# Performance work log

Hardware: AMD Instinct MI355X
Metric: run time of the kernel (lower is better)

## Reference

```python
import jax, jax.numpy as jnp
import numpy as np

BLOCK = 128
EPS = 1e-5

def _fp8_dequant_weight(w, s):
    # s: [out//128, in//128] per-block scales. Expand to full weight shape.
    sb = jnp.repeat(jnp.repeat(s, BLOCK, axis=0), BLOCK, axis=1)  # [out, in]
    # fake fp8 quantize: scale down, cast to e4m3, cast back, scale up
    wq = (w / sb).astype(jnp.float8_e4m3fn).astype(jnp.float32)
    return wq * sb

def _fp8_linear(x, w, s):
    return x @ _fp8_dequant_weight(w, s).T  # [N, out]

def _layernorm(h, gamma, beta):
    mu = jnp.mean(h, axis=-1, keepdims=True)
    var = jnp.mean(jnp.square(h - mu), axis=-1, keepdims=True)
    return (h - mu) * jax.lax.rsqrt(var + EPS) * gamma + beta

def setup_inputs() -> dict:
    key = jax.random.key(0)
    ks = jax.random.split(key, 4)
    H, LO, SO, N = 4096, 8192, 2048, 8192
    return {
        "x": jax.random.normal(ks[0], (N, H), dtype=jnp.float32),
        "w_a": jax.random.normal(ks[1], (LO, H), dtype=jnp.float32),
        "s_a": jnp.ones((LO // BLOCK, H // BLOCK), dtype=jnp.float32),
        "w_b": jax.random.normal(ks[2], (SO, H), dtype=jnp.float32),
        "s_b": jnp.ones((SO // BLOCK, H // BLOCK), dtype=jnp.float32),
        "w_proj": jax.random.normal(ks[3], (H, LO + SO), dtype=jnp.float32) * 0.01,
        "gamma": jnp.ones((H,), dtype=jnp.float32),
        "beta": jnp.zeros((H,), dtype=jnp.float32),
    }

def reference(x, w_a, s_a, w_b, s_b, w_proj, gamma, beta):
    a = _fp8_linear(x, w_a, s_a)          # [N, large_out]
    b = _fp8_linear(x, w_b, s_b)          # [N, small_out]
    combined = jnp.concatenate([a, b], axis=-1)
    h = combined @ w_proj.T               # [N, hidden]
    return _layernorm(h, gamma, beta)
```

## Files before the change

kernel.cpp:

```cpp
#include <hip/hip_runtime.h>


typedef unsigned int u32;
typedef unsigned short u16;
typedef __bf16 bf16x8 __attribute__((ext_vector_type(8)));
typedef float f32x4 __attribute__((ext_vector_type(4)));
typedef u16 u16x8 __attribute__((ext_vector_type(8)));

#define AS1 __attribute__((address_space(1)))
#define AS3 __attribute__((address_space(3)))

__device__ __forceinline__ u16 f2bf(float f) {
  u32 u = __float_as_uint(f);
  u32 r = (u + 0x7fffu + ((u >> 16) & 1u)) >> 16;
  return (u16)r;
}

__device__ __forceinline__ float q_e4m3(float v) {
  int p = __builtin_amdgcn_cvt_pk_fp8_f32(v, v, 0, false);
  return __builtin_amdgcn_cvt_f32_fp8(p, 0);
}

__device__ __forceinline__ void gload16(const void* g, void* l) {
  __builtin_amdgcn_global_load_lds((const AS1 u32*)g, (AS3 u32*)l, 16, 0, 0);
}

__global__ __launch_bounds__(256) void k_f32_to_bf16(
    const float* __restrict__ in, u16* __restrict__ out, long n) {
  long i0 = ((long)blockIdx.x * 256 + threadIdx.x) * 8;
  long stride = (long)gridDim.x * 256 * 8;
  for (long i = i0; i < n; i += stride) {
    float4 a = *(const float4*)(in + i);
    float4 b = *(const float4*)(in + i + 4);
    u16x8 o;
    o[0] = f2bf(a.x); o[1] = f2bf(a.y); o[2] = f2bf(a.z); o[3] = f2bf(a.w);
    o[4] = f2bf(b.x); o[5] = f2bf(b.y); o[6] = f2bf(b.z); o[7] = f2bf(b.w);
    *(u16x8*)(out + i) = o;
  }
}

__global__ __launch_bounds__(256) void k_quant_transpose(
    const float* __restrict__ w, const float* __restrict__ s,
    u16* __restrict__ oT, int J, int Kd, int sCols, long oStride, int oColOff) {
  __shared__ u16 tile[64][72];
  int j0 = blockIdx.x * 64;
  int k0 = blockIdx.y * 64;
  float sc = s[(j0 >> 7) * sCols + (k0 >> 7)];
  int t = threadIdx.x;
  int row = t >> 2, seg = t & 3;
  const float4* src = (const float4*)(w + (long)(j0 + row) * Kd + k0 + seg * 16);
  u16* dst = &tile[row][seg * 16];
#pragma unroll
  for (int ii = 0; ii < 4; ++ii) {
    float4 v = src[ii];
    dst[ii * 4 + 0] = f2bf(q_e4m3(v.x / sc) * sc);
    dst[ii * 4 + 1] = f2bf(q_e4m3(v.y / sc) * sc);
    dst[ii * 4 + 2] = f2bf(q_e4m3(v.z / sc) * sc);
    dst[ii * 4 + 3] = f2bf(q_e4m3(v.w / sc) * sc);
  }
  __syncthreads();
  int r = t >> 2, cs = t & 3;
  u16* op = oT + (long)(k0 + r) * oStride + oColOff + j0 + cs * 16;
  u16x8 o0, o1;
#pragma unroll
  for (int ii = 0; ii < 8; ++ii) o0[ii] = tile[cs * 16 + ii][r];
#pragma unroll
  for (int ii = 0; ii < 8; ++ii) o1[ii] = tile[cs * 16 + 8 + ii][r];
  *(u16x8*)op = o0;
  *(u16x8*)(op + 8) = o1;
}

template <bool OUT_BF16>
__global__ __launch_bounds__(512, 2) void k_gemm8(
    const u16* __restrict__ A, const u16* __restrict__ B, void* __restrict__ Cv,
    int M, int N, int K) {
  __shared__ u16 sA[2][256 * 64];
  __shared__ u16 sB[2][256 * 64];

  const int tid = threadIdx.x;
  const int lane = tid & 63;
  const int wave = tid >> 6;
  const int wr = wave >> 2, wc = wave & 3;

  const int nwg = gridDim.x;
  const int wg = blockIdx.x;
  const int wgs = (wg & 7) * (nwg >> 3) + (wg >> 3);
  const int nbn = N >> 8;
  const int m0 = (wgs / nbn) << 8;
  const int n0 = (wgs % nbn) << 8;
  const int NT = K >> 6;

  const int lrow = lane & 15;
  const int kslot = lane >> 4;
  const int st_row = lane >> 3;
  const int st_slot = lane & 7;
  const int st_src = ((st_slot ^ st_row) * 8);

  f32x4 acc[8][4] = {};

  auto stage = [&](const u16* __restrict__ G, int row0, u16* lds, int half,
                   int kt) {
#pragma unroll
    for (int r = 0; r < 2; ++r) {
      int row = half * 128 + r * 64 + wave * 8 + st_row;
      const u16* g = G + (long)(row0 + row) * K + kt * 64 + st_src;
      u16* l = lds + row * 64 + st_slot * 8;
      gload16(g, l);
    }
  };
  auto ldA = [&](const u16* sa, int mh, int m, int ks) -> bf16x8 {
    int row = wr * 128 + mh * 64 + m * 16 + lrow;
    int slot = (ks * 4 + kslot) ^ (row & 7);
    return *(const bf16x8*)(sa + row * 64 + slot * 8);
  };
  auto ldB = [&](const u16* sb, int n, int ks) -> bf16x8 {
    int row = wc * 64 + n * 16 + lrow;
    int slot = (ks * 4 + kslot) ^ (row & 7);
    return *(const bf16x8*)(sb + row * 64 + slot * 8);
  };

  stage(A, m0, sA[0], 0, 0);
  stage(A, m0, sA[0], 1, 0);
  stage(B, n0, sB[0], 0, 0);
  stage(B, n0, sB[0], 1, 0);
  if (NT > 1) {
    stage(B, n0, sB[1], 0, 1);
    stage(B, n0, sB[1], 1, 1);
    asm volatile("s_waitcnt vmcnt(4)" ::: "memory");
  } else {
    asm volatile("s_waitcnt vmcnt(0)" ::: "memory");
  }
  __builtin_amdgcn_s_barrier();

  bf16x8 b1r[2][2];
#pragma unroll
  for (int n = 0; n < 2; ++n)
#pragma unroll
    for (int ks = 0; ks < 2; ++ks) b1r[n][ks] = ldB(sB[0], n + 2, ks);

  for (int t = 0; t < NT; ++t) {
    const int p = t & 1;
    const u16* sa = sA[p];
    const u16* sb = sB[p];
    u16* saN = sA[p ^ 1];
    const u16* sbN = sB[p ^ 1];
    u16* sbC = sB[p];
    bf16x8 aT[4][2], aB[4][2], b0r[2][2];

#pragma unroll
    for (int m = 0; m < 4; ++m)
#pragma unroll
      for (int ks = 0; ks < 2; ++ks) aT[m][ks] = ldA(sa, 0, m, ks);
    if (t + 1 < NT) stage(A, m0, saN, 0, t + 1);
    __builtin_amdgcn_s_barrier();
    __builtin_amdgcn_s_setprio(1);
#pragma unroll
    for (int m = 0; m < 4; ++m)
#pragma unroll
      for (int n = 0; n < 2; ++n)
#pragma unroll
        for (int ks = 0; ks < 2; ++ks)
          acc[m][n + 2] = __builtin_amdgcn_mfma_f32_16x16x32_bf16(
              aT[m][ks], b1r[n][ks], acc[m][n + 2], 0, 0, 0);
    __builtin_amdgcn_s_setprio(0);
    __builtin_amdgcn_s_barrier();

#pragma unroll
    for (int n = 0; n < 2; ++n)
#pragma unroll
      for (int ks = 0; ks < 2; ++ks) b0r[n][ks] = ldB(sb, n, ks);
    if (t + 1 < NT) stage(A, m0, saN, 1, t + 1);
    __builtin_amdgcn_s_barrier();
    __builtin_amdgcn_s_setprio(1);
#pragma unroll
    for (int m = 0; m < 4; ++m)
#pragma unroll
      for (int n = 0; n < 2; ++n)
#pragma unroll
        for (int ks = 0; ks < 2; ++ks)
          acc[m][n] = __builtin_amdgcn_mfma_f32_16x16x32_bf16(
              aT[m][ks], b0r[n][ks], acc[m][n], 0, 0, 0);
    __builtin_amdgcn_s_setprio(0);
    __builtin_amdgcn_s_barrier();

#pragma unroll
    for (int m = 0; m < 4; ++m)
#pragma unroll
      for (int ks = 0; ks < 2; ++ks) aB[m][ks] = ldA(sa, 1, m, ks);
    if (t + 2 < NT) stage(B, n0, sbC, 0, t + 2);
    __builtin_amdgcn_s_barrier();
    __builtin_amdgcn_s_setprio(1);
#pragma unroll
    for (int m = 0; m < 4; ++m)
#pragma unroll
      for (int n = 0; n < 2; ++n)
#pragma unroll
        for (int ks = 0; ks < 2; ++ks)
          acc[4 + m][n + 2] = __builtin_amdgcn_mfma_f32_16x16x32_bf16(
              aB[m][ks], b1r[n][ks], acc[4 + m][n + 2], 0, 0, 0);
    __builtin_amdgcn_s_setprio(0);
    __builtin_amdgcn_s_barrier();

    if (t + 1 < NT) {
      if (t + 2 < NT)
        asm volatile("s_waitcnt vmcnt(6)" ::: "memory");
      else
        asm volatile("s_waitcnt vmcnt(4)" ::: "memory");
#pragma unroll
      for (int n = 0; n < 2; ++n)
#pragma unroll
        for (int ks = 0; ks < 2; ++ks) b1r[n][ks] = ldB(sbN, n + 2, ks);
    }
    if (t + 2 < NT) stage(B, n0, sbC, 1, t + 2);
    __builtin_amdgcn_s_barrier();
    __builtin_amdgcn_s_setprio(1);
#pragma unroll
    for (int m = 0; m < 4; ++m)
#pragma unroll
      for (int n = 0; n < 2; ++n)
#pragma unroll
        for (int ks = 0; ks < 2; ++ks)
          acc[4 + m][n] = __builtin_amdgcn_mfma_f32_16x16x32_bf16(
              aB[m][ks], b0r[n][ks], acc[4 + m][n], 0, 0, 0);
    __builtin_amdgcn_s_setprio(0);
    if (t + 2 < NT)
      asm volatile("s_waitcnt vmcnt(4)" ::: "memory");
    else
      asm volatile("s_waitcnt vmcnt(0)" ::: "memory");
    __builtin_amdgcn_s_barrier();
  }

  const int rb = m0 + wr * 128 + (lane >> 4) * 4;
  const int cb = n0 + wc * 64 + lrow;
#pragma unroll
  for (int mf = 0; mf < 8; ++mf) {
#pragma unroll
    for (int r = 0; r < 4; ++r) {
      const long rowoff = (long)(rb + mf * 16 + r) * N + cb;
#pragma unroll
      for (int n = 0; n < 4; ++n) {
        if (OUT_BF16)
          ((u16*)Cv)[rowoff + n * 16] = f2bf(acc[mf][n][r]);
        else
          ((float*)Cv)[rowoff + n * 16] = acc[mf][n][r];
      }
    }
  }
}

__global__ __launch_bounds__(256) void k_layernorm(
    float* __restrict__ h, const float* __restrict__ gamma,
    const float* __restrict__ beta) {
  const int H = 4096;
  float* p = h + (long)blockIdx.x * H;
  int t = threadIdx.x;
  float4 v[4];
  float sum = 0.f, sq = 0.f;
#pragma unroll
  for (int i = 0; i < 4; ++i) {
    v[i] = ((const float4*)p)[i * 256 + t];
    sum += v[i].x + v[i].y + v[i].z + v[i].w;
    sq += v[i].x * v[i].x + v[i].y * v[i].y + v[i].z * v[i].z + v[i].w * v[i].w;
  }
#pragma unroll
  for (int off = 32; off > 0; off >>= 1) {
    sum += __shfl_down(sum, off, 64);
    sq += __shfl_down(sq, off, 64);
  }
  __shared__ float ss[4], sg[4];
  if ((t & 63) == 0) { ss[t >> 6] = sum; sg[t >> 6] = sq; }
  __syncthreads();
  sum = ss[0] + ss[1] + ss[2] + ss[3];
  sq = sg[0] + sg[1] + sg[2] + sg[3];
  float mu = sum * (1.0f / H);
  float var = sq * (1.0f / H) - mu * mu;
  float rs = rsqrtf(var + 1e-5f);
#pragma unroll
  for (int i = 0; i < 4; ++i) {
    float4 g = ((const float4*)gamma)[i * 256 + t];
    float4 b = ((const float4*)beta)[i * 256 + t];
    float4 o;
    o.x = (v[i].x - mu) * rs * g.x + b.x;
    o.y = (v[i].y - mu) * rs * g.y + b.y;
    o.z = (v[i].z - mu) * rs * g.z + b.z;
    o.w = (v[i].w - mu) * rs * g.w + b.w;
    ((float4*)p)[i * 256 + t] = o;
  }
}

extern "C" void kernel_launch(void* const* d_in, const int* in_sizes, int n_in,
                              void* d_out, int out_size, void* d_ws,
                              size_t ws_size, hipStream_t stream) {
  const float* x      = (const float*)d_in[0];
  const float* w_a    = (const float*)d_in[1];
  const float* s_a    = (const float*)d_in[2];
  const float* w_b    = (const float*)d_in[3];
  const float* s_b    = (const float*)d_in[4];
  const float* w_proj = (const float*)d_in[5];
  const float* gamma  = (const float*)d_in[6];
  const float* beta   = (const float*)d_in[7];

  const int H = 4096, LO = 8192, SO = 2048, NR = 8192;
  const int KT = LO + SO;

  char* ws = (char*)d_ws;
  u16* xb   = (u16*)(ws);
  u16* wpb  = (u16*)(ws + 0x4000000L);
  u16* wqT  = (u16*)(ws + 0x9000000L);
  u16* weff = (u16*)(ws + 0xE000000L);
  float* h  = (float*)d_out;

  k_f32_to_bf16<<<2048, 256, 0, stream>>>(w_proj, wpb, (long)H * KT);
  k_quant_transpose<<<dim3(LO / 64, H / 64), 256, 0, stream>>>(
      w_a, s_a, wqT, LO, H, H / 128, (long)KT, 0);
  k_quant_transpose<<<dim3(SO / 64, H / 64), 256, 0, stream>>>(
      w_b, s_b, wqT, SO, H, H / 128, (long)KT, LO);

  k_gemm8<true><<<(H / 256) * (H / 256), 512, 0, stream>>>(
      wpb, wqT, (void*)weff, H, H, KT);

  k_f32_to_bf16<<<2048, 256, 0, stream>>>(x, xb, (long)NR * H);

  k_gemm8<false><<<(NR / 256) * (H / 256), 512, 0, stream>>>(
      xb, weff, (void*)h, NR, H, H);

  k_layernorm<<<NR, 256, 0, stream>>>(h, gamma, beta);
}
```

Baseline: 774.3 us.

## Unroll GEMM k-loop by two and reschedule B-fragment loads after MFMAs

New measurement: 723.4 us. 6.6% less time.

```diff
diff --git a/kernel.cpp b/kernel.cpp
--- a/kernel.cpp
+++ b/kernel.cpp
@@ -74,8 +74,8 @@
 __global__ __launch_bounds__(512, 2) void k_gemm8(
     const u16* __restrict__ A, const u16* __restrict__ B, void* __restrict__ Cv,
     int M, int N, int K) {
-  __shared__ u16 sA[2][256 * 64];
-  __shared__ u16 sB[2][256 * 64];
+  __shared__ u16 sAbuf[2][256 * 64];
+  __shared__ u16 sBbuf[2][256 * 64];
 
   const int tid = threadIdx.x;
   const int lane = tid & 63;
@@ -119,32 +119,10 @@
     return *(const bf16x8*)(sb + row * 64 + slot * 8);
   };
 
-  stage(A, m0, sA[0], 0, 0);
-  stage(A, m0, sA[0], 1, 0);
-  stage(B, n0, sB[0], 0, 0);
-  stage(B, n0, sB[0], 1, 0);
-  if (NT > 1) {
-    stage(B, n0, sB[1], 0, 1);
-    stage(B, n0, sB[1], 1, 1);
-    asm volatile("s_waitcnt vmcnt(4)" ::: "memory");
-  } else {
-    asm volatile("s_waitcnt vmcnt(0)" ::: "memory");
-  }
-  __builtin_amdgcn_s_barrier();
-
   bf16x8 b1r[2][2];
-#pragma unroll
-  for (int n = 0; n < 2; ++n)
-#pragma unroll
-    for (int ks = 0; ks < 2; ++ks) b1r[n][ks] = ldB(sB[0], n + 2, ks);
-
-  for (int t = 0; t < NT; ++t) {
-    const int p = t & 1;
-    const u16* sa = sA[p];
-    const u16* sb = sB[p];
-    u16* saN = sA[p ^ 1];
-    const u16* sbN = sB[p ^ 1];
-    u16* sbC = sB[p];
+
+  auto ktile = [&](int t, const u16* sa, const u16* sb, u16* saN,
+                   const u16* sbN) {
     bf16x8 aT[4][2], aB[4][2], b0r[2][2];
 
 #pragma unroll
@@ -153,6 +131,8 @@
       for (int ks = 0; ks < 2; ++ks) aT[m][ks] = ldA(sa, 0, m, ks);
     if (t + 1 < NT) stage(A, m0, saN, 0, t + 1);
     __builtin_amdgcn_s_barrier();
+    asm volatile("s_waitcnt lgkmcnt(0)");
+    __builtin_amdgcn_sched_barrier(0);
     __builtin_amdgcn_s_setprio(1);
 #pragma unroll
     for (int m = 0; m < 4; ++m)
@@ -171,6 +151,8 @@
       for (int ks = 0; ks < 2; ++ks) b0r[n][ks] = ldB(sb, n, ks);
     if (t + 1 < NT) stage(A, m0, saN, 1, t + 1);
     __builtin_amdgcn_s_barrier();
+    asm volatile("s_waitcnt lgkmcnt(0)");
+    __builtin_amdgcn_sched_barrier(0);
     __builtin_amdgcn_s_setprio(1);
 #pragma unroll
     for (int m = 0; m < 4; ++m)
@@ -187,8 +169,10 @@
     for (int m = 0; m < 4; ++m)
 #pragma unroll
       for (int ks = 0; ks < 2; ++ks) aB[m][ks] = ldA(sa, 1, m, ks);
-    if (t + 2 < NT) stage(B, n0, sbC, 0, t + 2);
-    __builtin_amdgcn_s_barrier();
+    if (t + 2 < NT) stage(B, n0, (u16*)sb, 0, t + 2);
+    __builtin_amdgcn_s_barrier();
+    asm volatile("s_waitcnt lgkmcnt(0)");
+    __builtin_amdgcn_sched_barrier(0);
     __builtin_amdgcn_s_setprio(1);
 #pragma unroll
     for (int m = 0; m < 4; ++m)
@@ -201,18 +185,15 @@
     __builtin_amdgcn_s_setprio(0);
     __builtin_amdgcn_s_barrier();
 
+    if (t + 2 < NT) stage(B, n0, (u16*)sb, 1, t + 2);
     if (t + 1 < NT) {
       if (t + 2 < NT)
-        asm volatile("s_waitcnt vmcnt(6)" ::: "memory");
+        asm volatile("s_waitcnt vmcnt(8)" ::: "memory");
       else
         asm volatile("s_waitcnt vmcnt(4)" ::: "memory");
-#pragma unroll
-      for (int n = 0; n < 2; ++n)
-#pragma unroll
-        for (int ks = 0; ks < 2; ++ks) b1r[n][ks] = ldB(sbN, n + 2, ks);
     }
-    if (t + 2 < NT) stage(B, n0, sbC, 1, t + 2);
-    __builtin_amdgcn_s_barrier();
+    __builtin_amdgcn_s_barrier();
+    __builtin_amdgcn_sched_barrier(0);
     __builtin_amdgcn_s_setprio(1);
 #pragma unroll
     for (int m = 0; m < 4; ++m)
@@ -223,11 +204,39 @@
           acc[4 + m][n] = __builtin_amdgcn_mfma_f32_16x16x32_bf16(
               aB[m][ks], b0r[n][ks], acc[4 + m][n], 0, 0, 0);
     __builtin_amdgcn_s_setprio(0);
+    if (t + 1 < NT) {
+#pragma unroll
+      for (int n = 0; n < 2; ++n)
+#pragma unroll
+        for (int ks = 0; ks < 2; ++ks) b1r[n][ks] = ldB(sbN, n + 2, ks);
+    }
     if (t + 2 < NT)
       asm volatile("s_waitcnt vmcnt(4)" ::: "memory");
     else
       asm volatile("s_waitcnt vmcnt(0)" ::: "memory");
     __builtin_amdgcn_s_barrier();
+  };
+
+  stage(A, m0, sAbuf[0], 0, 0);
+  stage(A, m0, sAbuf[0], 1, 0);
+  stage(B, n0, sBbuf[0], 0, 0);
+  stage(B, n0, sBbuf[0], 1, 0);
+  if (NT > 1) {
+    stage(B, n0, sBbuf[1], 0, 1);
+    stage(B, n0, sBbuf[1], 1, 1);
+    asm volatile("s_waitcnt vmcnt(4)" ::: "memory");
+  } else {
+    asm volatile("s_waitcnt vmcnt(0)" ::: "memory");
+  }
+  __builtin_amdgcn_s_barrier();
+#pragma unroll
+  for (int n = 0; n < 2; ++n)
+#pragma unroll
+    for (int ks = 0; ks < 2; ++ks) b1r[n][ks] = ldB(sBbuf[0], n + 2, ks);
+
+  for (int t = 0; t < NT; t += 2) {
+    ktile(t, sAbuf[0], sBbuf[0], sAbuf[1], sBbuf[1]);
+    ktile(t + 1, sAbuf[1], sBbuf[1], sAbuf[0], sBbuf[0]);
   }
 
   const int rb = m0 + wr * 128 + (lane >> 4) * 4;
```
